# Kernel tuning notes

Measured on AMD Instinct MI355X. Metric: run time of the kernel, lower is better.

## Reference

```python
import jax, jax.numpy as jnp
import numpy as np

N = 50000      # total nodes
E = 800000     # edges (before self loops)
B = 512        # graphs in batch
NODE_F = 9
GLOB_F = 4
IN_F = 13
H = 4          # heads
C = 16         # per-head channels (64 // 4)
HID = 64
NEG_SLOPE = 0.2


def setup_inputs() -> dict:
    key = jax.random.key(0)
    ks = jax.random.split(key, 32)
    inp = {}
    inp["node_feats"] = jax.random.normal(ks[0], (N, NODE_F), jnp.float32)
    inp["x_global_features"] = jax.random.normal(ks[1], (B, GLOB_F), jnp.float32)
    inp["edge_index"] = jax.random.randint(ks[2], (2, E), 0, N, jnp.int32)
    inp["batch_idx"] = jnp.sort(jax.random.randint(ks[3], (N,), 0, B, jnp.int32))
    dims = [IN_F, HID, HID]
    k = 4
    for l in range(3):
        s = 1.0 / np.sqrt(dims[l])
        inp[f"W{l}"] = jax.random.normal(ks[k], (dims[l], H * C), jnp.float32) * s; k += 1
        inp[f"att_src{l}"] = jax.random.normal(ks[k], (H, C), jnp.float32) * 0.1; k += 1
        inp[f"att_dst{l}"] = jax.random.normal(ks[k], (H, C), jnp.float32) * 0.1; k += 1
        inp[f"b{l}"] = jnp.zeros((H * C,), jnp.float32)
    mlp_dims = [(64, 64), (64, 64), (64, 64), (64, 1)]
    for i, (a, o) in enumerate(mlp_dims):
        inp[f"mlp_W{i}"] = jax.random.normal(ks[k], (a, o), jnp.float32) * (1.0 / np.sqrt(a)); k += 1
        inp[f"mlp_b{i}"] = jnp.zeros((o,), jnp.float32)
    return inp


def _gat_conv(x, src, dst, W, a_src, a_dst, bias, n):
    # h: [n, H, C]
    h = (x @ W).reshape(n, H, C)
    alpha_src = jnp.sum(h * a_src, axis=-1)   # [n, H]
    alpha_dst = jnp.sum(h * a_dst, axis=-1)   # [n, H]
    e = alpha_src[src] + alpha_dst[dst]       # [E', H]
    e = jax.nn.leaky_relu(e, NEG_SLOPE)
    # softmax over incoming edges per destination node (self loops guarantee >=1 edge)
    m = jax.ops.segment_max(e, dst, num_segments=n)
    e = jnp.exp(e - m[dst])
    s = jax.ops.segment_sum(e, dst, num_segments=n)
    alpha = e / s[dst]                        # [E', H]
    out = jax.ops.segment_sum(h[src] * alpha[:, :, None], dst, num_segments=n)
    return out.reshape(n, H * C) + bias


def _forward(node_feats, x_global_features,
             W0, att_src0, att_dst0, b0,
             W1, att_src1, att_dst1, b1,
             W2, att_src2, att_dst2, b2,
             mlp_W0, mlp_b0, mlp_W1, mlp_b1, mlp_W2, mlp_b2, mlp_W3, mlp_b3,
             edge_index, batch_idx):
    n = node_feats.shape[0]
    # concat per-graph global features onto each node
    x = jnp.concatenate([node_feats, x_global_features[batch_idx]], axis=1)  # [N, 13]
    loops = jnp.arange(n, dtype=edge_index.dtype)
    src = jnp.concatenate([edge_index[0], loops])
    dst = jnp.concatenate([edge_index[1], loops])
    x = jax.nn.relu(_gat_conv(x, src, dst, W0, att_src0, att_dst0, b0, n))
    x = jax.nn.relu(_gat_conv(x, src, dst, W1, att_src1, att_dst1, b1, n))
    x = _gat_conv(x, src, dst, W2, att_src2, att_dst2, b2, n)  # no act on last layer
    # scatter_mean over graphs
    sums = jax.ops.segment_sum(x, batch_idx, num_segments=B)
    cnt = jax.ops.segment_sum(jnp.ones((n,), x.dtype), batch_idx, num_segments=B)
    pooled = sums / jnp.clip(cnt, 1.0)[:, None]               # [B, 64]
    h = jax.nn.relu(pooled @ mlp_W0 + mlp_b0)
    h = jax.nn.relu(h @ mlp_W1 + mlp_b1)
    h = jax.nn.relu(h @ mlp_W2 + mlp_b2)
    out = h @ mlp_W3 + mlp_b3                                  # [B, 1]
    return out.reshape(-1)                                     # flatten -> [B]


def reference(node_feats, x_global_features,
              W0, att_src0, att_dst0, b0,
              W1, att_src1, att_dst1, b1,
              W2, att_src2, att_dst2, b2,
              mlp_W0, mlp_b0, mlp_W1, mlp_b1, mlp_W2, mlp_b2, mlp_W3, mlp_b3,
              edge_index, batch_idx):
    return _forward(node_feats, x_global_features,
                    W0, att_src0, att_dst0, b0,
                    W1, att_src1, att_dst1, b1,
                    W2, att_src2, att_dst2, b2,
                    mlp_W0, mlp_b0, mlp_W1, mlp_b1, mlp_W2, mlp_b2, mlp_W3, mlp_b3,
                    edge_index, batch_idx)
```

## Files before the change

kernel.cpp:

```cpp
#include <hip/hip_runtime.h>

#define GAT_H 4
#define GAT_HC 64
#define NEG_SLOPE 0.2f
#define DB 128
#define NBMAX 512
#define CHUNK 4096
#define EPT 16

__device__ __forceinline__ float lrelu(float x) { return x >= 0.f ? x : NEG_SLOPE * x; }

template <int K, bool CONCAT>
__global__ __launch_bounds__(256) void gemm_attn(
    const float* __restrict__ x, const float* __restrict__ nf,
    const float* __restrict__ gf, const int* __restrict__ batch,
    const float* __restrict__ W,
    const float* __restrict__ att_s, const float* __restrict__ att_d,
    float* __restrict__ h, float* __restrict__ asrc, float* __restrict__ adst,
    int N, int nwaves)
{
    int lane = threadIdx.x & 63;
    int wid = blockIdx.x * 4 + __builtin_amdgcn_readfirstlane(threadIdx.x >> 6);

    float w[K];
    #pragma unroll
    for (int k = 0; k < K; ++k) w[k] = W[k * 64 + lane];
    float as_c = att_s[lane];
    float ad_c = att_d[lane];

    for (int row = wid; row < N; row += nwaves) {
        float acc = 0.f;
        if (CONCAT) {
            #pragma unroll
            for (int k = 0; k < 9; ++k) acc = fmaf(nf[row * 9 + k], w[k], acc);
            int b = batch[row];
            #pragma unroll
            for (int k = 0; k < 4; ++k) acc = fmaf(gf[b * 4 + k], w[9 + k], acc);
        } else {
            #pragma unroll
            for (int k = 0; k < K; ++k) acc = fmaf(x[(size_t)row * K + k], w[k], acc);
        }
        h[(unsigned)row * 64u + (unsigned)lane] = acc;
        float vs = acc * as_c;
        float vd = acc * ad_c;
        #pragma unroll
        for (int off = 8; off; off >>= 1) { vs += __shfl_xor(vs, off); vd += __shfl_xor(vd, off); }
        if ((lane & 15) == 0) {
            asrc[row * GAT_H + (lane >> 4)] = vs;
            adst[row * GAT_H + (lane >> 4)] = vd;
        }
    }
}


__global__ __launch_bounds__(256) void zero_small(unsigned* __restrict__ bin_cnt,
                                                  unsigned* __restrict__ bin_fill)
{
    int t = threadIdx.x;
    bin_cnt[t] = 0; bin_cnt[t + 256] = 0;
    bin_fill[t] = 0; bin_fill[t + 256] = 0;
}

__global__ __launch_bounds__(256) void hist_bins(const int* __restrict__ dst,
                                                 unsigned* __restrict__ bin_cnt, int E)
{
    __shared__ unsigned lh[NBMAX];
    int t = threadIdx.x;
    lh[t] = 0; lh[t + 256] = 0;
    __syncthreads();
    for (int e = blockIdx.x * 256 + t; e < E; e += gridDim.x * 256)
        atomicAdd(&lh[((unsigned)dst[e]) >> 7], 1u);
    __syncthreads();
    unsigned v = lh[t];       if (v) atomicAdd(&bin_cnt[t], v);
    v = lh[t + 256];          if (v) atomicAdd(&bin_cnt[t + 256], v);
}

__global__ __launch_bounds__(256) void scan_bins(const unsigned* __restrict__ bin_cnt,
                                                 unsigned* __restrict__ bin_base,
                                                 int* __restrict__ indptr,
                                                 int nb, int N, int E)
{
    __shared__ unsigned buf[NBMAX];
    int t = threadIdx.x;
    buf[t] = (t < nb) ? bin_cnt[t] : 0u;
    buf[t + 256] = (t + 256 < nb) ? bin_cnt[t + 256] : 0u;
    __syncthreads();
    for (int off = 1; off < NBMAX; off <<= 1) {
        unsigned a = 0, b = 0;
        if (t >= off) a = buf[t - off];
        b = buf[t + 256 - off];
        __syncthreads();
        buf[t] += a; buf[t + 256] += b;
        __syncthreads();
    }
    if (t == 0) { bin_base[0] = 0; indptr[N] = E; }
    if (t < nb) bin_base[t + 1] = buf[t];
    if (t + 256 < nb) bin_base[t + 257] = buf[t + 256];
}

__global__ __launch_bounds__(256) void bin_scatter(const int* __restrict__ src,
                                                   const int* __restrict__ dst,
                                                   const unsigned* __restrict__ bin_base,
                                                   unsigned* __restrict__ bin_fill,
                                                   unsigned* __restrict__ binned, int E)
{
    __shared__ unsigned lh[NBMAX];
    __shared__ int goff[NBMAX];
    __shared__ unsigned sorted[CHUNK];
    int t = threadIdx.x;
    lh[t] = 0; lh[t + 256] = 0;
    __syncthreads();
    int e0 = blockIdx.x * CHUNK;

    unsigned pk[EPT]; int bn[EPT]; unsigned rk[EPT];
    #pragma unroll
    for (int i = 0; i < EPT; ++i) {
        int e = e0 + i * 256 + t;
        bn[i] = -1;
        if (e < E) {
            unsigned d = (unsigned)dst[e];
            pk[i] = (d << 16) | (unsigned)src[e];
            bn[i] = (int)(d >> 7);
            rk[i] = atomicAdd(&lh[bn[i]], 1u);
        }
    }
    __syncthreads();
    unsigned c0 = lh[t], c1 = lh[t + 256];
    for (int off = 1; off < NBMAX; off <<= 1) {
        unsigned a = 0, b = 0;
        if (t >= off) a = lh[t - off];
        b = lh[t + 256 - off];
        __syncthreads();
        lh[t] += a; lh[t + 256] += b;
        __syncthreads();
    }
    unsigned x0 = lh[t] - c0, x1 = lh[t + 256] - c1;
    if (c0) { unsigned g = atomicAdd(&bin_fill[t], c0);
              goff[t] = (int)(bin_base[t] + g) - (int)x0; }
    if (c1) { unsigned g = atomicAdd(&bin_fill[t + 256], c1);
              goff[t + 256] = (int)(bin_base[t + 256] + g) - (int)x1; }
    lh[t] = x0; lh[t + 256] = x1;
    __syncthreads();
    #pragma unroll
    for (int i = 0; i < EPT; ++i)
        if (bn[i] >= 0) sorted[lh[bn[i]] + rk[i]] = pk[i];
    __syncthreads();
    int T = min(CHUNK, E - e0);
    for (int j = t; j < T; j += 256) {
        unsigned p = sorted[j];
        binned[goff[p >> 23] + j] = p;
    }
}

__global__ __launch_bounds__(256) void bin_finalize(const unsigned* __restrict__ binned,
                                                    const unsigned* __restrict__ bin_base,
                                                    int* __restrict__ csr_src,
                                                    int* __restrict__ indptr, int N)
{
    __shared__ unsigned lh[DB];
    __shared__ unsigned fill[DB];
    int t = threadIdx.x, b = blockIdx.x;
    unsigned base = bin_base[b];
    unsigned cnt = bin_base[b + 1] - base;
    if (t < DB) lh[t] = 0;
    __syncthreads();
    for (unsigned i = t; i < cnt; i += 256)
        atomicAdd(&lh[(binned[base + i] >> 16) & (DB - 1)], 1u);
    __syncthreads();
    unsigned c0 = (t < DB) ? lh[t] : 0;
    for (int off = 1; off < DB; off <<= 1) {
        unsigned a = 0;
        if (t >= off && t < DB) a = lh[t - off];
        __syncthreads();
        if (t < DB) lh[t] += a;
        __syncthreads();
    }
    if (t < DB) {
        unsigned excl = lh[t] - c0;
        int d = b * DB + t;
        if (d < N) indptr[d] = (int)(base + excl);
        fill[t] = excl;
    }
    __syncthreads();
    for (unsigned i = t; i < cnt; i += 256) {
        unsigned p = binned[base + i];
        unsigned pos = atomicAdd(&fill[(p >> 16) & (DB - 1)], 1u);
        csr_src[base + pos] = (int)(p & 0xFFFFu);
    }
}

template <bool RELU>
__global__ __launch_bounds__(256) void aggregate(
    const float* __restrict__ h, const float* __restrict__ asrc,
    const float* __restrict__ adst, const int* __restrict__ indptr,
    const int* __restrict__ csr_src, const float* __restrict__ bias,
    float* __restrict__ xout, int N, int nwaves)
{
    int lane = threadIdx.x & 63;
    int wid = blockIdx.x * 4 + __builtin_amdgcn_readfirstlane(threadIdx.x >> 6);
    unsigned h16 = (unsigned)(lane >> 4);
    float bias_c = bias[lane];

    for (int node = wid; node < N; node += nwaves) {
        int beg = __builtin_amdgcn_readfirstlane(indptr[node]);
        int end = __builtin_amdgcn_readfirstlane(indptr[node + 1]);
        unsigned un = (unsigned)node;

        float adst_n = adst[un * 4u + h16];
        float p0 = __expf(lrelu(asrc[un * 4u + h16] + adst_n));
        float sacc = p0;
        float acc = h[un * 64u + (unsigned)lane] * p0;

        int e = beg;
        for (; e + 8 <= end; e += 8) {
            int s[8]; float a[8], hv[8];
            #pragma unroll
            for (int i = 0; i < 8; ++i) s[i] = csr_src[e + i];
            #pragma unroll
            for (int i = 0; i < 8; ++i) a[i] = asrc[(unsigned)s[i] * 4u + h16];
            #pragma unroll
            for (int i = 0; i < 8; ++i) hv[i] = h[(unsigned)s[i] * 64u + (unsigned)lane];
            #pragma unroll
            for (int i = 0; i < 8; ++i) {
                float p = __expf(lrelu(a[i] + adst_n));
                sacc += p;
                acc = fmaf(hv[i], p, acc);
            }
        }
        for (; e + 2 <= end; e += 2) {
            int s0 = csr_src[e], s1 = csr_src[e + 1];
            float a0 = asrc[(unsigned)s0 * 4u + h16];
            float a1 = asrc[(unsigned)s1 * 4u + h16];
            float h0 = h[(unsigned)s0 * 64u + (unsigned)lane];
            float h1 = h[(unsigned)s1 * 64u + (unsigned)lane];
            float pa = __expf(lrelu(a0 + adst_n));
            float pb = __expf(lrelu(a1 + adst_n));
            sacc += pa + pb;
            acc = fmaf(h0, pa, acc);
            acc = fmaf(h1, pb, acc);
        }
        if (e < end) {
            int s = csr_src[e];
            float p = __expf(lrelu(asrc[(unsigned)s * 4u + h16] + adst_n));
            sacc += p;
            acc = fmaf(h[(unsigned)s * 64u + (unsigned)lane], p, acc);
        }

        float o = acc / sacc + bias_c;
        if (RELU) o = fmaxf(o, 0.f);
        xout[un * 64u + (unsigned)lane] = o;
    }
}

__global__ void pool_mlp(const float* __restrict__ x, const int* __restrict__ batch, int N,
                         const float* __restrict__ W0, const float* __restrict__ b0,
                         const float* __restrict__ W1, const float* __restrict__ b1,
                         const float* __restrict__ W2, const float* __restrict__ b2,
                         const float* __restrict__ W3, const float* __restrict__ b3,
                         float* __restrict__ out)
{
    __shared__ int bounds[2];
    __shared__ float red[4][64];
    __shared__ float hb[64];
    int b = blockIdx.x, t = threadIdx.x;

    if (t < 2) {
        int target = b + t;
        int lo = 0, hi = N;
        while (lo < hi) {
            int mid = (lo + hi) >> 1;
            if (batch[mid] < target) lo = mid + 1; else hi = mid;
        }
        bounds[t] = lo;
    }
    __syncthreads();
    int beg = bounds[0], end = bounds[1];

    int c = t & 63, w = t >> 6;
    float sum = 0.f;
    for (int n = beg + w; n < end; n += 4) sum += x[(size_t)n * 64 + c];
    red[w][c] = sum;
    __syncthreads();
    if (t < 64) {
        float v = red[0][t] + red[1][t] + red[2][t] + red[3][t];
        float cb = fmaxf((float)(end - beg), 1.0f);
        hb[t] = v / cb;
    }
    __syncthreads();

    float v0 = 0.f;
    if (t < 64) {
        v0 = b0[t];
        for (int k = 0; k < 64; ++k) v0 = fmaf(hb[k], W0[k * 64 + t], v0);
        v0 = fmaxf(v0, 0.f);
    }
    __syncthreads(); if (t < 64) hb[t] = v0; __syncthreads();
    if (t < 64) {
        v0 = b1[t];
        for (int k = 0; k < 64; ++k) v0 = fmaf(hb[k], W1[k * 64 + t], v0);
        v0 = fmaxf(v0, 0.f);
    }
    __syncthreads(); if (t < 64) hb[t] = v0; __syncthreads();
    if (t < 64) {
        v0 = b2[t];
        for (int k = 0; k < 64; ++k) v0 = fmaf(hb[k], W2[k * 64 + t], v0);
        v0 = fmaxf(v0, 0.f);
    }
    __syncthreads(); if (t < 64) hb[t] = v0; __syncthreads();
    if (t < 64) {
        float r = hb[t] * W3[t];
        #pragma unroll
        for (int off = 32; off; off >>= 1) r += __shfl_xor(r, off);
        if (t == 0) out[b] = r + b3[0];
    }
}

extern "C" void kernel_launch(void* const* d_in, const int* in_sizes, int n_in,
                              void* d_out, int out_size, void* d_ws, size_t ws_size,
                              hipStream_t stream)
{
    const float* node_feats = (const float*)d_in[0];
    const float* glob       = (const float*)d_in[1];
    const int*   edge_index = (const int*)d_in[2];
    const int*   batch      = (const int*)d_in[3];
    const float* W[3]  = {(const float*)d_in[4],  (const float*)d_in[8],  (const float*)d_in[12]};
    const float* As[3] = {(const float*)d_in[5],  (const float*)d_in[9],  (const float*)d_in[13]};
    const float* Ad[3] = {(const float*)d_in[6],  (const float*)d_in[10], (const float*)d_in[14]};
    const float* Bi[3] = {(const float*)d_in[7],  (const float*)d_in[11], (const float*)d_in[15]};
    const float* mW0 = (const float*)d_in[16]; const float* mb0 = (const float*)d_in[17];
    const float* mW1 = (const float*)d_in[18]; const float* mb1 = (const float*)d_in[19];
    const float* mW2 = (const float*)d_in[20]; const float* mb2 = (const float*)d_in[21];
    const float* mW3 = (const float*)d_in[22]; const float* mb3 = (const float*)d_in[23];
    float* out = (float*)d_out;

    int N = in_sizes[0] / 9;
    int E = in_sizes[2] / 2;
    int B = in_sizes[1] / 4;
    const int* esrc = edge_index;
    const int* edst = edge_index + E;
    int nb = (N + DB - 1) / DB;

    char* ws = (char*)d_ws;
    size_t off = 0;
    auto alloc = [&](size_t bytes) -> void* {
        void* p = ws + off;
        off = (off + bytes + 255) & ~(size_t)255;
        return p;
    };
    float*    hbuf     = (float*)alloc((size_t)N * 64 * 4);
    float*    xbuf     = (float*)alloc((size_t)N * 64 * 4);
    float*    asrc     = (float*)alloc((size_t)N * GAT_H * 4);
    float*    adst     = (float*)alloc((size_t)N * GAT_H * 4);
    int*      indptr   = (int*)alloc((size_t)(N + 1) * 4);
    int*      csr_src  = (int*)alloc((size_t)E * 4);
    unsigned* binned   = (unsigned*)alloc((size_t)E * 4);
    unsigned* bin_cnt  = (unsigned*)alloc(NBMAX * 4);
    unsigned* bin_base = (unsigned*)alloc((NBMAX + 1) * 4);
    unsigned* bin_fill = (unsigned*)alloc(NBMAX * 4);
    (void)ws_size;

    zero_small<<<1, 256, 0, stream>>>(bin_cnt, bin_fill);
    hist_bins<<<400, 256, 0, stream>>>(edst, bin_cnt, E);
    scan_bins<<<1, 256, 0, stream>>>(bin_cnt, bin_base, indptr, nb, N, E);
    bin_scatter<<<(E + CHUNK - 1) / CHUNK, 256, 0, stream>>>(esrc, edst, bin_base, bin_fill,
                                                             binned, E);
    bin_finalize<<<nb, 256, 0, stream>>>(binned, bin_base, csr_src, indptr, N);

    const int gemmBlocks = 1024;
    const int aggBlocks = 6250;
    gemm_attn<13, true><<<gemmBlocks, 256, 0, stream>>>(nullptr, node_feats, glob, batch,
                                                        W[0], As[0], Ad[0], hbuf, asrc, adst,
                                                        N, gemmBlocks * 4);
    aggregate<true><<<aggBlocks, 256, 0, stream>>>(hbuf, asrc, adst, indptr, csr_src, Bi[0],
                                                   xbuf, N, aggBlocks * 4);
    gemm_attn<64, false><<<gemmBlocks, 256, 0, stream>>>(xbuf, nullptr, nullptr, nullptr,
                                                         W[1], As[1], Ad[1], hbuf, asrc, adst,
                                                         N, gemmBlocks * 4);
    aggregate<true><<<aggBlocks, 256, 0, stream>>>(hbuf, asrc, adst, indptr, csr_src, Bi[1],
                                                   xbuf, N, aggBlocks * 4);
    gemm_attn<64, false><<<gemmBlocks, 256, 0, stream>>>(xbuf, nullptr, nullptr, nullptr,
                                                         W[2], As[2], Ad[2], hbuf, asrc, adst,
                                                         N, gemmBlocks * 4);
    aggregate<false><<<aggBlocks, 256, 0, stream>>>(hbuf, asrc, adst, indptr, csr_src, Bi[2],
                                                    xbuf, N, aggBlocks * 4);

    pool_mlp<<<B, 256, 0, stream>>>(xbuf, batch, N,
                                    mW0, mb0, mW1, mb1, mW2, mb2, mW3, mb3, out);
}
```

Measured before the change: 208.9 us.

## Store projected node features in fp16 and scalarize neighbor index loads

The projected features h are now stored as half precision, which halves the bytes of the random gather that dominates the aggregation kernels. Neighbor indices are made wave-uniform with readfirstlane, and attention scores are fetched as a single float4 per neighbor instead of one float per head. The cost is lower precision in the aggregated features, which could push results outside tolerance. The gathered fp16 rows are also only 128 bytes, so memory access efficiency per lane changes.

```diff
diff --git a/kernel.cpp b/kernel.cpp
--- a/kernel.cpp
+++ b/kernel.cpp
@@ -1,4 +1,5 @@
 #include <hip/hip_runtime.h>
+#include <hip/hip_fp16.h>
 
 #define GAT_H 4
 #define GAT_HC 64
@@ -16,7 +17,7 @@
     const float* __restrict__ gf, const int* __restrict__ batch,
     const float* __restrict__ W,
     const float* __restrict__ att_s, const float* __restrict__ att_d,
-    float* __restrict__ h, float* __restrict__ asrc, float* __restrict__ adst,
+    __half* __restrict__ h, float* __restrict__ asrc, float* __restrict__ adst,
     int N, int nwaves)
 {
     int lane = threadIdx.x & 63;
@@ -40,7 +41,7 @@
             #pragma unroll
             for (int k = 0; k < K; ++k) acc = fmaf(x[(size_t)row * K + k], w[k], acc);
         }
-        h[(unsigned)row * 64u + (unsigned)lane] = acc;
+        h[(unsigned)row * 64u + (unsigned)lane] = __float2half(acc);
         float vs = acc * as_c;
         float vd = acc * ad_c;
         #pragma unroll
@@ -191,7 +192,7 @@
 
 template <bool RELU>
 __global__ __launch_bounds__(256) void aggregate(
-    const float* __restrict__ h, const float* __restrict__ asrc,
+    const __half* __restrict__ h, const float* __restrict__ asrc,
     const float* __restrict__ adst, const int* __restrict__ indptr,
     const int* __restrict__ csr_src, const float* __restrict__ bias,
     float* __restrict__ xout, int N, int nwaves)
@@ -209,17 +210,22 @@
         float adst_n = adst[un * 4u + h16];
         float p0 = __expf(lrelu(asrc[un * 4u + h16] + adst_n));
         float sacc = p0;
-        float acc = h[un * 64u + (unsigned)lane] * p0;
+        float acc = __half2float(h[un * 64u + (unsigned)lane]) * p0;
 
         int e = beg;
         for (; e + 8 <= end; e += 8) {
             int s[8]; float a[8], hv[8];
             #pragma unroll
-            for (int i = 0; i < 8; ++i) s[i] = csr_src[e + i];
-            #pragma unroll
-            for (int i = 0; i < 8; ++i) a[i] = asrc[(unsigned)s[i] * 4u + h16];
-            #pragma unroll
-            for (int i = 0; i < 8; ++i) hv[i] = h[(unsigned)s[i] * 64u + (unsigned)lane];
+            for (int i = 0; i < 8; ++i) s[i] = __builtin_amdgcn_readfirstlane(csr_src[e + i]);
+            #pragma unroll
+            for (int i = 0; i < 8; ++i) {
+                float4 av = *reinterpret_cast<const float4*>(asrc + (unsigned)s[i] * 4u);
+                a[i] = (h16 < 2u) ? (h16 == 0u ? av.x : av.y)
+                                  : (h16 == 2u ? av.z : av.w);
+            }
+            #pragma unroll
+            for (int i = 0; i < 8; ++i)
+                hv[i] = __half2float(h[(unsigned)s[i] * 64u + (unsigned)lane]);
             #pragma unroll
             for (int i = 0; i < 8; ++i) {
                 float p = __expf(lrelu(a[i] + adst_n));
@@ -228,11 +234,16 @@
             }
         }
         for (; e + 2 <= end; e += 2) {
-            int s0 = csr_src[e], s1 = csr_src[e + 1];
-            float a0 = asrc[(unsigned)s0 * 4u + h16];
-            float a1 = asrc[(unsigned)s1 * 4u + h16];
-            float h0 = h[(unsigned)s0 * 64u + (unsigned)lane];
-            float h1 = h[(unsigned)s1 * 64u + (unsigned)lane];
+            int s0 = __builtin_amdgcn_readfirstlane(csr_src[e]);
+            int s1 = __builtin_amdgcn_readfirstlane(csr_src[e + 1]);
+            float4 av0 = *reinterpret_cast<const float4*>(asrc + (unsigned)s0 * 4u);
+            float4 av1 = *reinterpret_cast<const float4*>(asrc + (unsigned)s1 * 4u);
+            float a0 = (h16 < 2u) ? (h16 == 0u ? av0.x : av0.y)
+                                  : (h16 == 2u ? av0.z : av0.w);
+            float a1 = (h16 < 2u) ? (h16 == 0u ? av1.x : av1.y)
+                                  : (h16 == 2u ? av1.z : av1.w);
+            float h0 = __half2float(h[(unsigned)s0 * 64u + (unsigned)lane]);
+            float h1 = __half2float(h[(unsigned)s1 * 64u + (unsigned)lane]);
             float pa = __expf(lrelu(a0 + adst_n));
             float pb = __expf(lrelu(a1 + adst_n));
             sacc += pa + pb;
@@ -240,10 +251,13 @@
             acc = fmaf(h1, pb, acc);
         }
         if (e < end) {
-            int s = csr_src[e];
-            float p = __expf(lrelu(asrc[(unsigned)s * 4u + h16] + adst_n));
+            int s = __builtin_amdgcn_readfirstlane(csr_src[e]);
+            float4 av = *reinterpret_cast<const float4*>(asrc + (unsigned)s * 4u);
+            float a = (h16 < 2u) ? (h16 == 0u ? av.x : av.y)
+                                 : (h16 == 2u ? av.z : av.w);
+            float p = __expf(lrelu(a + adst_n));
             sacc += p;
-            acc = fmaf(h[(unsigned)s * 64u + (unsigned)lane], p, acc);
+            acc = fmaf(__half2float(h[(unsigned)s * 64u + (unsigned)lane]), p, acc);
         }
 
         float o = acc / sacc + bias_c;
@@ -347,7 +361,7 @@
         off = (off + bytes + 255) & ~(size_t)255;
         return p;
     };
-    float*    hbuf     = (float*)alloc((size_t)N * 64 * 4);
+    __half*   hbuf     = (__half*)alloc((size_t)N * 64 * 2);
     float*    xbuf     = (float*)alloc((size_t)N * 64 * 4);
     float*    asrc     = (float*)alloc((size_t)N * GAT_H * 4);
     float*    adst     = (float*)alloc((size_t)N * GAT_H * 4);
```

After: 265.8 us. +27.2%, slower.
